# Optimization experiments

Hardware: AMD Instinct MI355X
Metric: run time of the kernel (lower is better)

The kernel has to match this reference:

```python
import math
import jax, jax.numpy as jnp
import numpy as np
from jax import lax

RADIUS = 3
KSIZE = 2 * RADIUS + 1  # 7
TOP_K = 8
SINKHORN_ITERS = 5


def _box_sum(x, h_axis, w_axis):
    # sum pooling with same padding over spatial axes
    wd = [1] * x.ndim
    wd[h_axis] = KSIZE
    wd[w_axis] = KSIZE
    pads = [(0, 0)] * x.ndim
    pads[h_axis] = (RADIUS, RADIUS)
    pads[w_axis] = (RADIUS, RADIUS)
    return lax.reduce_window(x, 0.0, lax.add, tuple(wd), (1,) * x.ndim, pads)


def geo_validate(src_pos, cand_pos, H, W):
    # src_pos [B,N,2], cand_pos [B,N,K,2] -> score [B,N,K]
    B, N, K, _ = cand_pos.shape
    src = src_pos.reshape(B, H, W, 1, 2)
    cand = cand_pos.reshape(B, H, W, K, 2)
    disp = cand - src  # [B,H,W,K,2]
    # count_include_pad=False -> divide by number of valid (in-bounds) taps
    cnt = _box_sum(jnp.ones((1, H, W, 1, 1), disp.dtype), 1, 2)
    mean = _box_sum(disp, 1, 2) / cnt
    mean_sq = _box_sum(disp * disp, 1, 2) / cnt
    var = jnp.clip(mean_sq - mean * mean, 0.0)
    total_var = var.sum(-1).reshape(B, N, K)
    return 1.0 / (1.0 + 100.0 * total_var)


def optimal_transport(scores, dustbin):
    B, M, N = scores.shape
    row = jnp.broadcast_to(dustbin, (B, M, 1))
    col = jnp.broadcast_to(dustbin, (B, 1, N))
    corner = jnp.zeros((B, 1, 1), scores.dtype)
    Z = jnp.concatenate([jnp.concatenate([scores, row], 2),
                         jnp.concatenate([col, corner], 2)], 1)  # [B,M+1,N+1]
    norm = -math.log(M + N)
    log_mu = jnp.full((M + 1,), norm, scores.dtype).at[M].set(math.log(N) + norm)
    log_nu = jnp.full((N + 1,), norm, scores.dtype).at[N].set(math.log(M) + norm)
    log_mu = jnp.broadcast_to(log_mu, (B, M + 1))
    log_nu = jnp.broadcast_to(log_nu, (B, N + 1))

    def body(_, uv):
        u, v = uv
        u = log_mu - jax.nn.logsumexp(Z + v[:, None, :], axis=2)
        v = log_nu - jax.nn.logsumexp(Z + u[:, :, None], axis=1)
        return (u, v)

    u0 = jnp.zeros((B, M + 1), scores.dtype)
    v0 = jnp.zeros((B, N + 1), scores.dtype)
    u, v = lax.fori_loop(0, SINKHORN_ITERS, body, (u0, v0))
    log_assign = Z + u[:, :, None] + v[:, None, :]
    return log_assign[:, :M, :N]


def solve_weighted_affine(src_pts, dst_pts, weights):
    # src/dst [B,N,2], weights [B,N,1] -> H_mat [B,3,3]
    B, N, _ = src_pts.shape
    w = weights[..., 0]
    w = w / jnp.clip(w.sum(1, keepdims=True), 1e-6)
    x, y = src_pts[..., 0], src_pts[..., 1]
    one = jnp.ones_like(x)
    zero = jnp.zeros_like(x)
    row_x = jnp.stack([x, y, one, zero, zero, zero], -1)   # [B,N,6]
    row_y = jnp.stack([zero, zero, zero, x, y, one], -1)
    A = jnp.concatenate([row_x, row_y], 1)                 # [B,2N,6]
    b = jnp.concatenate([dst_pts[..., 0], dst_pts[..., 1]], 1)[..., None]
    wd = jnp.concatenate([w, w], 1)[..., None]             # [B,2N,1]
    Aw = A * wd
    AtWA = jnp.einsum('bni,bnj->bij', Aw, A) + 1e-4 * jnp.eye(6, dtype=A.dtype)
    AtWb = jnp.einsum('bni,bnk->bik', Aw, b)
    p = jnp.linalg.solve(AtWA, AtWb)[..., 0]               # [B,6]
    a_, b_, c_, d_, e_, f_ = [p[:, i] for i in range(6)]
    z = jnp.zeros_like(a_)
    o = jnp.ones_like(a_)
    return jnp.stack([a_, b_, c_, d_, e_, f_, z, z, o], -1).reshape(B, 3, 3)


def matcher_forward(feat_A, feat_B, pos_A, pos_B, dustbin_score, geo_weight,
                    current_temp, H, W):
    B, N, C = feat_A.shape
    temp = current_temp[0]
    nA = feat_A / jnp.clip(jnp.linalg.norm(feat_A, axis=-1, keepdims=True), 1e-12)
    nB = feat_B / jnp.clip(jnp.linalg.norm(feat_B, axis=-1, keepdims=True), 1e-12)
    scores = jnp.einsum('bnc,bmc->bnm', nA, nB) / temp      # [B,N,N]
    log_assign = optimal_transport(scores, dustbin_score[0])
    ot_prob = jnp.exp(log_assign)
    topk_vals, topk_idx = lax.top_k(ot_prob, TOP_K)          # [B,N,K]
    bidx = jnp.arange(B)[:, None, None]
    topk_pos = pos_B[bidx, topk_idx]                         # [B,N,K,2]
    geo = geo_validate(pos_A, topk_pos, H, W)                # [B,N,K]
    gw = jnp.clip(geo_weight[0], 0.0, 2.0)
    combined = topk_vals + gw * geo
    soft = jax.nn.softmax(combined / temp, axis=-1)
    refined_warp = (topk_pos * soft[..., None]).sum(2)       # [B,N,2]
    conf = (soft * topk_vals).sum(-1, keepdims=True)         # [B,N,1]
    H_mat = solve_weighted_affine(pos_A, refined_warp, conf)
    return refined_warp, conf, H_mat


def setup_inputs() -> dict:
    key = jax.random.key(0)
    kA, kB, kP = jax.random.split(key, 3)
    B, H, W, C = 2, 64, 64, 128
    N = H * W
    feat_A = jax.random.normal(kA, (B, N, C), jnp.float32)
    feat_B = jax.random.normal(kB, (B, N, C), jnp.float32)
    # dense grid positions, normalized to [0,1]
    ys, xs = jnp.meshgrid(jnp.arange(H, dtype=jnp.float32),
                          jnp.arange(W, dtype=jnp.float32), indexing='ij')
    grid = jnp.stack([xs, ys], -1).reshape(1, N, 2) / float(max(H, W))
    pos_A = jnp.broadcast_to(grid, (B, N, 2))
    pos_B = pos_A + 0.01 * jax.random.normal(kP, (B, N, 2), jnp.float32)
    return {
        'feat_A': feat_A, 'feat_B': feat_B,
        'pos_A': pos_A, 'pos_B': pos_B,
        'dustbin_score': jnp.full((1,), -1.0, jnp.float32),
        'geo_weight': jnp.full((1,), 0.5, jnp.float32),
        'current_temp': jnp.full((1,), 0.1, jnp.float32),
        'H': H, 'W': W,
    }


def reference(feat_A, feat_B, pos_A, pos_B, dustbin_score, geo_weight,
              current_temp, H, W):
    return matcher_forward(feat_A, feat_B, pos_A, pos_B, dustbin_score,
                           geo_weight, current_temp, H, W)
```

## Files before the change

kernel.cpp:

```cpp
#include <hip/hip_runtime.h>
#include <math.h>

#define UVS 4104

#define OFF_ZU    33554432ul
#define OFF_WV    (OFF_ZU + 2*UVS)
#define OFF_RN    (OFF_WV + 2*UVS)
#define OFF_PARTS (OFF_RN + 16384)
#define OFF_TKV   (OFF_PARTS + 2097152)
#define OFF_TKP   (OFF_TKV + 65536)
#define OFF_DP    (OFF_TKP + 131072)
#define OFF_GEO   (OFF_DP + 131072)
#define OFF_SUM   (OFF_GEO + 65536)

#define EXPC    0.0001220703125f
#define HALFC   0.5f

#define PLANE   1048576

typedef __attribute__((ext_vector_type(8))) short bf16x8;
typedef __attribute__((ext_vector_type(4))) float f32x4;

static __device__ __forceinline__ unsigned f2bf(float x) {
    unsigned u = __float_as_uint(x);
    return (u + 0x7FFFu + ((u >> 16) & 1u)) >> 16;
}
static __device__ __forceinline__ float bf2f(unsigned h) { return __uint_as_float(h << 16); }

__global__ __launch_bounds__(256) void init_kernel(float* __restrict__ wv)
{
    int i = blockIdx.x * 256 + threadIdx.x;
    if (i < 2 * UVS) wv[i] = 1.0f;
}

__global__ __launch_bounds__(256) void norms_kernel(
    const float* __restrict__ fA, const float* __restrict__ fB, float* __restrict__ rn)
{
    int t = threadIdx.x;
    int rowg = blockIdx.x * 4 + (t >> 6);
    int lane = t & 63;
    const float* f = (rowg < 8192) ? fA : fB;
    int r = rowg & 8191;
    float x0 = f[(size_t)r * 128 + lane];
    float x1 = f[(size_t)r * 128 + 64 + lane];
    float s = x0 * x0 + x1 * x1;
    #pragma unroll
    for (int off = 32; off > 0; off >>= 1) s += __shfl_xor(s, off, 64);
    if (lane == 0) rn[rowg] = 1.f / fmaxf(sqrtf(s), 1e-12f);
}

__global__ __launch_bounds__(256) void pack_kernel(
    const float* __restrict__ fA, const float* __restrict__ fB, short* __restrict__ pk)
{
    int gt = blockIdx.x * 256 + threadIdx.x;
    int tensor = gt >> 17;
    int t = gt & 131071;
    int fr = t & 15;
    int kc = (t >> 4) & 15;
    int rb = (t >> 8) & 255;
    int b  = t >> 16;
    const float* src = tensor ? fB : fA;
    const float* p = src + ((size_t)(b * 4096 + rb * 16 + fr)) * 128 + kc * 8;
    float4 v0 = *(const float4*)p;
    float4 v1 = *(const float4*)(p + 4);
    float el[8] = {v0.x, v0.y, v0.z, v0.w, v1.x, v1.y, v1.z, v1.w};
    unsigned h[8], l[8];
    #pragma unroll
    for (int e = 0; e < 8; e++) { h[e] = f2bf(el[e]); l[e] = f2bf(el[e] - bf2f(h[e])); }
    uint4 hw = make_uint4(h[0] | (h[1] << 16), h[2] | (h[3] << 16),
                          h[4] | (h[5] << 16), h[6] | (h[7] << 16));
    uint4 lw = make_uint4(l[0] | (l[1] << 16), l[2] | (l[3] << 16),
                          l[4] | (l[5] << 16), l[6] | (l[7] << 16));
    size_t off = ((size_t)(b * 256 + rb)) * 2048 + kc * 128 + fr * 8;
    short* hi = pk + (size_t)tensor * 2 * PLANE;
    *(uint4*)(hi + off) = hw;
    *(uint4*)(hi + PLANE + off) = lw;
}

__global__ __launch_bounds__(256) void gemm_mfma(
    const short* __restrict__ pk, const float* __restrict__ rn,
    const float* __restrict__ temp, float* __restrict__ E0)
{
    __shared__ short Bs[16384];
    int b = blockIdx.z;
    int i0 = blockIdx.y * 64, j0 = blockIdx.x * 64;
    int t = threadIdx.x;
    int wave = t >> 6, lane = t & 63;
    int fr = lane & 15;
    int quad = lane >> 4;

    const short* gBhi = pk + 2 * (size_t)PLANE + ((size_t)(b * 256 + (j0 >> 4))) * 2048;
    const short* gBlo = gBhi + PLANE;
    #pragma unroll
    for (int c = 0; c < 4; c++) {
        int ch = c * 256 + t;
        *(uint4*)&Bs[ch * 8]        = *(const uint4*)(gBhi + ch * 8);
        *(uint4*)&Bs[8192 + ch * 8] = *(const uint4*)(gBlo + ch * 8);
    }

    const short* Abase_hi = pk + ((size_t)(b * 256 + (i0 >> 4) + wave)) * 2048;
    const short* Abase_lo = Abase_hi + PLANE;
    bf16x8 ah[4], al[4];
    #pragma unroll
    for (int s = 0; s < 4; s++) {
        ah[s] = *(const bf16x8*)(Abase_hi + s * 512 + lane * 8);
        al[s] = *(const bf16x8*)(Abase_lo + s * 512 + lane * 8);
    }
    __syncthreads();

    f32x4 acc[4] = {f32x4{0,0,0,0}, f32x4{0,0,0,0}, f32x4{0,0,0,0}, f32x4{0,0,0,0}};
    #pragma unroll
    for (int s = 0; s < 4; s++) {
        int lo = s * 512 + lane * 8;
        #pragma unroll
        for (int nb = 0; nb < 4; nb++) {
            bf16x8 bh = *(const bf16x8*)&Bs[nb * 2048 + lo];
            bf16x8 bl = *(const bf16x8*)&Bs[8192 + nb * 2048 + lo];
            acc[nb] = __builtin_amdgcn_mfma_f32_16x16x32_bf16(ah[s], bh, acc[nb], 0, 0, 0);
            acc[nb] = __builtin_amdgcn_mfma_f32_16x16x32_bf16(al[s], bh, acc[nb], 0, 0, 0);
            acc[nb] = __builtin_amdgcn_mfma_f32_16x16x32_bf16(ah[s], bl, acc[nb], 0, 0, 0);
        }
    }

    float invt = 1.f / temp[0];
    int m0 = i0 + wave * 16 + quad * 4;
    float ra[4];
    #pragma unroll
    for (int rr = 0; rr < 4; rr++) ra[rr] = rn[b * 4096 + m0 + rr] * invt;
    #pragma unroll
    for (int nb = 0; nb < 4; nb++) {
        int col = j0 + nb * 16 + fr;
        float rbv = rn[8192 + b * 4096 + col];
        #pragma unroll
        for (int rr = 0; rr < 4; rr++)
            E0[((size_t)(b * 4096 + m0 + rr)) * 4096 + col] = __expf(acc[nb][rr] * (ra[rr] * rbv));
    }
}

__global__ __launch_bounds__(256) void sink_fused(
    const float* __restrict__ E0, float* __restrict__ zu, const float* __restrict__ wv,
    const float* __restrict__ dbp, float* __restrict__ parts)
{
    int b = blockIdx.z;
    int t = threadIdx.x;
    int wave = t >> 6, lane = t & 63;
    int chb = blockIdx.x;
    const float* wb = wv + b * UVS;
    float edb = __expf(dbp[0]);
    __shared__ float S[4][4096];

    if (chb == 0 && wave == 0) {
        float sv = 0.f;
        #pragma unroll
        for (int c = 0; c < 16; c++) {
            f32x4 w4 = *(const f32x4*)(wb + lane * 4 + c * 256);
            sv += (w4.x + w4.y) + (w4.z + w4.w);
        }
        #pragma unroll
        for (int off = 32; off > 0; off >>= 1) sv += __shfl_xor(sv, off, 64);
        if (lane == 0) zu[b * UVS + 4096] = HALFC / (edb * sv + wb[4096]);
    }

    float dtail = edb * wb[4096];
    f32x4 cacc[16];
    #pragma unroll
    for (int c = 0; c < 16; c++) cacc[c] = f32x4{0, 0, 0, 0};

    const float* Eb = E0 + ((size_t)b << 24);
    int base = lane * 4;

    for (int r = 0; r < 4; r++) {
        int row = chb * 16 + wave * 4 + r;
        const float* Erow = Eb + ((size_t)row << 12);
        f32x4 x4[16];
        #pragma unroll
        for (int c = 0; c < 16; c++) x4[c] = *(const f32x4*)(Erow + base + c * 256);
        f32x4 rs4 = f32x4{0, 0, 0, 0};
        #pragma unroll
        for (int c = 0; c < 16; c++) {
            f32x4 w4 = *(const f32x4*)(wb + base + c * 256);
            rs4 += x4[c] * w4;
        }
        float rs = (rs4.x + rs4.y) + (rs4.z + rs4.w);
        #pragma unroll
        for (int off = 32; off > 0; off >>= 1) rs += __shfl_xor(rs, off, 64);
        float zi = EXPC / (rs + dtail);
        if (lane == 0) zu[b * UVS + row] = zi;
        #pragma unroll
        for (int c = 0; c < 16; c++) cacc[c] += x4[c] * zi;
    }

    #pragma unroll
    for (int c = 0; c < 16; c++) *(f32x4*)&S[wave][base + c * 256] = cacc[c];
    __syncthreads();
    float* pp = parts + ((size_t)(b * 256 + chb)) * 4096;
    #pragma unroll
    for (int k = 0; k < 16; k++) {
        int col = t + k * 256;
        pp[col] = (S[0][col] + S[1][col]) + (S[2][col] + S[3][col]);
    }
}

__global__ __launch_bounds__(256) void sink_vB(
    const float* __restrict__ parts, const float* __restrict__ zu,
    float* __restrict__ wv, const float* __restrict__ dbp)
{
    int b = blockIdx.z;
    int t = threadIdx.x;
    float edb = __expf(dbp[0]);
    if (blockIdx.x < 64) {
        int col = blockIdx.x * 64 + (t & 63);
        int grp = t >> 6;
        float s = 0.f;
        #pragma unroll 8
        for (int ch = grp * 64; ch < grp * 64 + 64; ch++)
            s += parts[((size_t)(b * 256 + ch)) * 4096 + col];
        __shared__ float red[4][64];
        red[grp][t & 63] = s;
        __syncthreads();
        if (grp == 0) {
            float tot = (red[0][t] + red[1][t]) + (red[2][t] + red[3][t]);
            tot += edb * zu[b * UVS + 4096];
            wv[b * UVS + col] = EXPC / tot;
        }
    } else {
        __shared__ float red2[256];
        float s = 0.f;
        for (int i = t; i < 4096; i += 256) s += zu[b * UVS + i];
        red2[t] = s; __syncthreads();
        for (int off = 128; off > 0; off >>= 1) {
            if (t < off) red2[t] += red2[t + off];
            __syncthreads();
        }
        if (t == 0)
            wv[b * UVS + 4096] = HALFC / (edb * red2[0] + zu[b * UVS + 4096]);
    }
}

#define FCMPSWAP(a, b) { float _mx = fmaxf(a, b), _mn = fminf(a, b); (a) = _mx; (b) = _mn; }
__global__ __launch_bounds__(256) void topk_kernel(
    const float* __restrict__ E0, const float* __restrict__ zu, const float* __restrict__ wv,
    const float* __restrict__ posA, const float* __restrict__ posB,
    float* __restrict__ tkv, float* __restrict__ tkp, float* __restrict__ dp)
{
    int wave = threadIdx.x >> 6;
    int lane = threadIdx.x & 63;
    int row = blockIdx.x * 4 + wave;
    int b = row >> 12; int i = row & 4095;
    const float* Erow = E0 + (size_t)row * 4096;
    const float* wb = wv + b * UVS;

    __shared__ unsigned long long cand[4][64];
    __shared__ int ccnt[4];
    if (lane == 0) ccnt[wave] = 0;

    f32x4 q[16];
    #pragma unroll
    for (int c = 0; c < 16; c++) {
        int j = c * 256 + lane * 4;
        f32x4 x = *(const f32x4*)(Erow + j);
        f32x4 w = *(const f32x4*)(wb + j);
        q[c] = x * w;
    }
    __builtin_amdgcn_sched_barrier(0);

    float s[8] = {0, 0, 0, 0, 0, 0, 0, 0};
    #pragma unroll
    for (int c = 0; c < 16; c++) {
        float el[4] = {q[c].x, q[c].y, q[c].z, q[c].w};
        #pragma unroll
        for (int e = 0; e < 4; e++) {
            float xv = el[e];
            s[7] = __builtin_amdgcn_fmed3f(s[6], s[7], xv);
            s[6] = __builtin_amdgcn_fmed3f(s[5], s[6], xv);
            s[5] = __builtin_amdgcn_fmed3f(s[4], s[5], xv);
            s[4] = __builtin_amdgcn_fmed3f(s[3], s[4], xv);
            s[3] = __builtin_amdgcn_fmed3f(s[2], s[3], xv);
            s[2] = __builtin_amdgcn_fmed3f(s[1], s[2], xv);
            s[1] = __builtin_amdgcn_fmed3f(s[0], s[1], xv);
            s[0] = fmaxf(s[0], xv);
        }
    }

    #pragma unroll
    for (int st = 0; st < 6; st++) {
        int off = 1 << st;
        float o[8];
        #pragma unroll
        for (int r = 0; r < 8; r++) o[r] = __shfl_xor(s[r], off, 64);
        float m[8];
        #pragma unroll
        for (int r = 0; r < 8; r++) m[r] = fmaxf(s[r], o[7 - r]);
        FCMPSWAP(m[0], m[4]); FCMPSWAP(m[1], m[5]); FCMPSWAP(m[2], m[6]); FCMPSWAP(m[3], m[7]);
        FCMPSWAP(m[0], m[2]); FCMPSWAP(m[1], m[3]); FCMPSWAP(m[4], m[6]); FCMPSWAP(m[5], m[7]);
        FCMPSWAP(m[0], m[1]); FCMPSWAP(m[2], m[3]); FCMPSWAP(m[4], m[5]); FCMPSWAP(m[6], m[7]);
        #pragma unroll
        for (int r = 0; r < 8; r++) s[r] = m[r];
    }
    float t8 = s[7];

    __syncthreads();

    #pragma unroll
    for (int c = 0; c < 16; c++) {
        float el[4] = {q[c].x, q[c].y, q[c].z, q[c].w};
        #pragma unroll
        for (int e = 0; e < 4; e++) {
            if (el[e] >= t8) {
                int j = c * 256 + lane * 4 + e;
                unsigned long long key =
                    ((unsigned long long)__float_as_uint(el[e]) << 32) | (unsigned)(4095 - j);
                int slot = atomicAdd(&ccnt[wave], 1);
                if (slot < 64) cand[wave][slot] = key;
            }
        }
    }
    __syncthreads();

    int cnt = ccnt[wave]; if (cnt > 64) cnt = 64;
    if (lane < cnt) {
        unsigned long long my = cand[wave][lane];
        int rank = 0;
        for (int j2 = 0; j2 < cnt; j2++) rank += (cand[wave][j2] > my) ? 1 : 0;
        if (rank < 8) {
            int idx = 4095 - (int)(my & 0xFFFFFFFFu);
            float candv = __uint_as_float((unsigned)(my >> 32));
            float val = candv * zu[b * UVS + i];
            float px = posB[((size_t)(b * 4096 + idx)) * 2 + 0];
            float py = posB[((size_t)(b * 4096 + idx)) * 2 + 1];
            float ax = posA[((size_t)(b * 4096 + i)) * 2 + 0];
            float ay = posA[((size_t)(b * 4096 + i)) * 2 + 1];
            size_t base = ((size_t)(b * 4096 + i)) * 8 + rank;
            tkv[base] = val;
            tkp[base * 2 + 0] = px; tkp[base * 2 + 1] = py;
            dp[((size_t)((b * 8 + rank) * 2 + 0)) * 4096 + i] = px - ax;
            dp[((size_t)((b * 8 + rank) * 2 + 1)) * 4096 + i] = py - ay;
        }
    }
}

__global__ __launch_bounds__(256) void geo_kernel(
    const float* __restrict__ dp, float* __restrict__ geo)
{
    int tid = blockIdx.x * 256 + threadIdx.x;
    int n = tid & 4095; int bk = tid >> 12;
    int b = bk >> 3; int k = bk & 7;
    int h = n >> 6, w = n & 63;
    const float* dpx = dp + ((size_t)(bk * 2 + 0)) * 4096;
    const float* dpy = dp + ((size_t)(bk * 2 + 1)) * 4096;
    float sx = 0, sy = 0, sxx = 0, syy = 0, cnt = 0;
    #pragma unroll
    for (int dy = -3; dy <= 3; dy++) {
        int hh = h + dy; if ((unsigned)hh >= 64u) continue;
        #pragma unroll
        for (int dx = -3; dx <= 3; dx++) {
            int ww = w + dx; if ((unsigned)ww >= 64u) continue;
            int nn = (hh << 6) + ww;
            float vx = dpx[nn], vy = dpy[nn];
            sx += vx; sy += vy; sxx += vx * vx; syy += vy * vy; cnt += 1.f;
        }
    }
    float inv = 1.f / cnt;
    float mx = sx * inv, my = sy * inv;
    float varx = fmaxf(sxx * inv - mx * mx, 0.f);
    float vary = fmaxf(syy * inv - my * my, 0.f);
    geo[((size_t)(b * 4096 + n)) * 8 + k] = 1.f / (1.f + 100.f * (varx + vary));
}

__global__ __launch_bounds__(256) void refine_kernel(
    const float* __restrict__ tkv, const float* __restrict__ geo,
    const float* __restrict__ tkp, const float* __restrict__ gwp,
    const float* __restrict__ tpp, float* __restrict__ out)
{
    int tid = blockIdx.x * 256 + threadIdx.x;
    float gw = fminf(fmaxf(gwp[0], 0.f), 2.f);
    float invt = 1.f / tpp[0];
    size_t base = (size_t)tid * 8;
    float cb[8], vv[8];
    float mx = -INFINITY;
    #pragma unroll
    for (int k = 0; k < 8; k++) { vv[k] = tkv[base + k]; cb[k] = vv[k] + gw * geo[base + k]; mx = fmaxf(mx, cb[k]); }
    float e[8], se = 0;
    #pragma unroll
    for (int k = 0; k < 8; k++) { e[k] = __expf((cb[k] - mx) * invt); se += e[k]; }
    float wx = 0, wy = 0, cf = 0; float inv = 1.f / se;
    #pragma unroll
    for (int k = 0; k < 8; k++) {
        float s = e[k] * inv;
        wx += s * tkp[(base + k) * 2 + 0];
        wy += s * tkp[(base + k) * 2 + 1];
        cf += s * vv[k];
    }
    out[(size_t)tid * 2 + 0] = wx;
    out[(size_t)tid * 2 + 1] = wy;
    out[16384 + tid] = cf;
}

__global__ __launch_bounds__(256) void affine_reduce(
    const float* __restrict__ posA, const float* __restrict__ out, double* __restrict__ sums)
{
    int b = blockIdx.x; int t = threadIdx.x;
    double acc[12] = {0,0,0,0,0,0,0,0,0,0,0,0};
    for (int n = t; n < 4096; n += 256) {
        size_t idx = (size_t)b * 4096 + n;
        float x = posA[idx * 2], y = posA[idx * 2 + 1];
        float dx = out[idx * 2], dy = out[idx * 2 + 1];
        float c = out[16384 + idx];
        double cd = (double)c;
        double cx = cd * x, cy = cd * y;
        acc[0] += cx * x;  acc[1] += cx * y;  acc[2] += cy * y;
        acc[3] += cx;      acc[4] += cy;      acc[5] += cd;
        acc[6] += cx * dx; acc[7] += cy * dx; acc[8] += cd * dx;
        acc[9] += cx * dy; acc[10] += cy * dy; acc[11] += cd * dy;
    }
    __shared__ double red[256];
    for (int s = 0; s < 12; s++) {
        red[t] = acc[s]; __syncthreads();
        for (int off = 128; off > 0; off >>= 1) {
            if (t < off) red[t] += red[t + off];
            __syncthreads();
        }
        if (t == 0) sums[b * 12 + s] = red[0];
        __syncthreads();
    }
}

__global__ void affine_solve(const double* __restrict__ sums, float* __restrict__ out)
{
    int t = threadIdx.x;
    if (t >= 2) return;
    int b = t;
    const double* s = sums + b * 12;
    double den = s[5] > 1e-6 ? s[5] : 1e-6;
    double g00 = s[0] / den + 1e-4, g01 = s[1] / den, g02 = s[3] / den;
    double g11 = s[2] / den + 1e-4, g12 = s[4] / den;
    double g22 = s[5] / den + 1e-4;
    double bx0 = s[6] / den, bx1 = s[7] / den, bx2 = s[8] / den;
    double by0 = s[9] / den, by1 = s[10] / den, by2 = s[11] / den;
    double c00 = g11 * g22 - g12 * g12;
    double c01 = g02 * g12 - g01 * g22;
    double c02 = g01 * g12 - g02 * g11;
    double det = g00 * c00 + g01 * c01 + g02 * c02;
    double id = 1.0 / det;
    double i00 = c00 * id, i01 = c01 * id, i02 = c02 * id;
    double i11 = (g00 * g22 - g02 * g02) * id, i12 = (g01 * g02 - g00 * g12) * id;
    double i22 = (g00 * g11 - g01 * g01) * id;
    double a_ = i00 * bx0 + i01 * bx1 + i02 * bx2;
    double b_ = i01 * bx0 + i11 * bx1 + i12 * bx2;
    double c_ = i02 * bx0 + i12 * bx1 + i22 * bx2;
    double d_ = i00 * by0 + i01 * by1 + i02 * by2;
    double e_ = i01 * by0 + i11 * by1 + i12 * by2;
    double f_ = i02 * by0 + i12 * by1 + i22 * by2;
    float* o = out + 24576 + b * 9;
    o[0] = (float)a_; o[1] = (float)b_; o[2] = (float)c_;
    o[3] = (float)d_; o[4] = (float)e_; o[5] = (float)f_;
    o[6] = 0.f; o[7] = 0.f; o[8] = 1.f;
}

extern "C" void kernel_launch(void* const* d_in, const int* in_sizes, int n_in,
                              void* d_out, int out_size, void* d_ws, size_t ws_size,
                              hipStream_t stream) {
    const float* fA = (const float*)d_in[0];
    const float* fB = (const float*)d_in[1];
    const float* pA = (const float*)d_in[2];
    const float* pB = (const float*)d_in[3];
    const float* db = (const float*)d_in[4];
    const float* gw = (const float*)d_in[5];
    const float* tp = (const float*)d_in[6];

    float* ws    = (float*)d_ws;
    float* out   = (float*)d_out;
    float* E0    = ws;
    float* zu    = ws + OFF_ZU;
    float* wv    = ws + OFF_WV;
    float* rn    = ws + OFF_RN;
    float* parts = ws + OFF_PARTS;
    short* pk    = (short*)(ws + OFF_PARTS);
    float* tkv   = ws + OFF_TKV;
    float* tkp   = ws + OFF_TKP;
    float* dp    = ws + OFF_DP;
    float* geo   = ws + OFF_GEO;
    double* sums = (double*)(ws + OFF_SUM);

    init_kernel<<<33, 256, 0, stream>>>(wv);
    norms_kernel<<<4096, 256, 0, stream>>>(fA, fB, rn);
    pack_kernel<<<1024, 256, 0, stream>>>(fA, fB, pk);
    gemm_mfma<<<dim3(64, 64, 2), 256, 0, stream>>>(pk, rn, tp, E0);

    for (int it = 0; it < 5; it++) {
        sink_fused<<<dim3(256, 1, 2), 256, 0, stream>>>(E0, zu, wv, db, parts);
        sink_vB<<<dim3(65, 1, 2), 256, 0, stream>>>(parts, zu, wv, db);
    }

    topk_kernel<<<2048, 256, 0, stream>>>(E0, zu, wv, pA, pB, tkv, tkp, dp);
    geo_kernel<<<256, 256, 0, stream>>>(dp, geo);
    refine_kernel<<<32, 256, 0, stream>>>(tkv, geo, tkp, gw, tp, out);
    affine_reduce<<<2, 256, 0, stream>>>(pA, out, sums);
    affine_solve<<<1, 64, 0, stream>>>(sums, out);
}
```

Baseline: 323.2 us.

## Double-buffer row loads in sinkhorn kernel and split top-k rows across whole block

The sinkhorn row-scaling kernel now prefetches the next row's 16 vector loads into a second register buffer while computing the current row, overlapping global loads with the dot product and accumulation. The top-k kernel now assigns one row per 256-thread block instead of one row per wave. Each thread scans 16 elements instead of 64, and per-wave top-8 lists are merged in shared memory to find the threshold. This shortens the serial per-thread sort chain and raises parallelism, at the cost of more register pressure in sinkhorn, four times as many top-k blocks, and an extra block-level barrier and merge step.

Result: slower. 358.6 us (+11.0%).

```diff
diff --git a/kernel.cpp b/kernel.cpp
--- a/kernel.cpp
+++ b/kernel.cpp
@@ -168,27 +168,44 @@
 
     const float* Eb = E0 + ((size_t)b << 24);
     int base = lane * 4;
-
-    for (int r = 0; r < 4; r++) {
-        int row = chb * 16 + wave * 4 + r;
-        const float* Erow = Eb + ((size_t)row << 12);
-        f32x4 x4[16];
-        #pragma unroll
-        for (int c = 0; c < 16; c++) x4[c] = *(const f32x4*)(Erow + base + c * 256);
-        f32x4 rs4 = f32x4{0, 0, 0, 0};
-        #pragma unroll
-        for (int c = 0; c < 16; c++) {
-            f32x4 w4 = *(const f32x4*)(wb + base + c * 256);
-            rs4 += x4[c] * w4;
-        }
-        float rs = (rs4.x + rs4.y) + (rs4.z + rs4.w);
-        #pragma unroll
-        for (int off = 32; off > 0; off >>= 1) rs += __shfl_xor(rs, off, 64);
-        float zi = EXPC / (rs + dtail);
-        if (lane == 0) zu[b * UVS + row] = zi;
-        #pragma unroll
-        for (int c = 0; c < 16; c++) cacc[c] += x4[c] * zi;
-    }
+    int row0 = chb * 16 + wave * 4;
+
+    f32x4 xa[16], xb[16];
+    {
+        const float* Er = Eb + ((size_t)row0 << 12);
+        #pragma unroll
+        for (int c = 0; c < 16; c++) xa[c] = *(const f32x4*)(Er + base + c * 256);
+    }
+
+#define SINK_ROW(BUF, NXT, ROW, PREF)                                          \
+    {                                                                          \
+        if (PREF) {                                                            \
+            const float* Ern = Eb + ((size_t)((ROW) + 1) << 12);               \
+            _Pragma("unroll")                                                  \
+            for (int c = 0; c < 16; c++)                                       \
+                NXT[c] = *(const f32x4*)(Ern + base + c * 256);                \
+        }                                                                      \
+        __builtin_amdgcn_sched_barrier(0);                                     \
+        f32x4 rs4 = f32x4{0, 0, 0, 0};                                         \
+        _Pragma("unroll")                                                      \
+        for (int c = 0; c < 16; c++) {                                         \
+            f32x4 w4 = *(const f32x4*)(wb + base + c * 256);                   \
+            rs4 += BUF[c] * w4;                                                \
+        }                                                                      \
+        float rs = (rs4.x + rs4.y) + (rs4.z + rs4.w);                          \
+        _Pragma("unroll")                                                      \
+        for (int off = 32; off > 0; off >>= 1) rs += __shfl_xor(rs, off, 64);  \
+        float zi = EXPC / (rs + dtail);                                        \
+        if (lane == 0) zu[b * UVS + (ROW)] = zi;                               \
+        _Pragma("unroll")                                                      \
+        for (int c = 0; c < 16; c++) cacc[c] += BUF[c] * zi;                   \
+    }
+
+    SINK_ROW(xa, xb, row0 + 0, 1)
+    SINK_ROW(xb, xa, row0 + 1, 1)
+    SINK_ROW(xa, xb, row0 + 2, 1)
+    SINK_ROW(xb, xa, row0 + 3, 0)
+#undef SINK_ROW
 
     #pragma unroll
     for (int c = 0; c < 16; c++) *(f32x4*)&S[wave][base + c * 256] = cacc[c];
@@ -243,21 +260,23 @@
     const float* __restrict__ posA, const float* __restrict__ posB,
     float* __restrict__ tkv, float* __restrict__ tkp, float* __restrict__ dp)
 {
-    int wave = threadIdx.x >> 6;
-    int lane = threadIdx.x & 63;
-    int row = blockIdx.x * 4 + wave;
+    int row = blockIdx.x;
+    int t = threadIdx.x;
+    int wave = t >> 6, lane = t & 63;
     int b = row >> 12; int i = row & 4095;
     const float* Erow = E0 + (size_t)row * 4096;
     const float* wb = wv + b * UVS;
 
-    __shared__ unsigned long long cand[4][64];
-    __shared__ int ccnt[4];
-    if (lane == 0) ccnt[wave] = 0;
-
-    f32x4 q[16];
-    #pragma unroll
-    for (int c = 0; c < 16; c++) {
-        int j = c * 256 + lane * 4;
+    __shared__ float sv32[32];
+    __shared__ float t8s;
+    __shared__ unsigned long long cand[64];
+    __shared__ int ccnt;
+    if (t == 0) ccnt = 0;
+
+    f32x4 q[4];
+    #pragma unroll
+    for (int c = 0; c < 4; c++) {
+        int j = t * 4 + c * 1024;
         f32x4 x = *(const f32x4*)(Erow + j);
         f32x4 w = *(const f32x4*)(wb + j);
         q[c] = x * w;
@@ -266,7 +285,7 @@
 
     float s[8] = {0, 0, 0, 0, 0, 0, 0, 0};
     #pragma unroll
-    for (int c = 0; c < 16; c++) {
+    for (int c = 0; c < 4; c++) {
         float el[4] = {q[c].x, q[c].y, q[c].z, q[c].w};
         #pragma unroll
         for (int e = 0; e < 4; e++) {
@@ -297,31 +316,46 @@
         #pragma unroll
         for (int r = 0; r < 8; r++) s[r] = m[r];
     }
-    float t8 = s[7];
-
+    if (lane == 0) {
+        #pragma unroll
+        for (int r = 0; r < 8; r++) sv32[wave * 8 + r] = s[r];
+    }
     __syncthreads();
 
-    #pragma unroll
-    for (int c = 0; c < 16; c++) {
+    if (t < 32) {
+        float my = sv32[t];
+        int rank = 0;
+        #pragma unroll
+        for (int k = 0; k < 32; k++) {
+            float vk = sv32[k];
+            rank += (vk > my || (vk == my && k < t)) ? 1 : 0;
+        }
+        if (rank == 7) t8s = my;
+    }
+    __syncthreads();
+    float t8 = t8s;
+
+    #pragma unroll
+    for (int c = 0; c < 4; c++) {
         float el[4] = {q[c].x, q[c].y, q[c].z, q[c].w};
         #pragma unroll
         for (int e = 0; e < 4; e++) {
             if (el[e] >= t8) {
-                int j = c * 256 + lane * 4 + e;
+                int j = t * 4 + c * 1024 + e;
                 unsigned long long key =
                     ((unsigned long long)__float_as_uint(el[e]) << 32) | (unsigned)(4095 - j);
-                int slot = atomicAdd(&ccnt[wave], 1);
-                if (slot < 64) cand[wave][slot] = key;
+                int slot = atomicAdd(&ccnt, 1);
+                if (slot < 64) cand[slot] = key;
             }
         }
     }
     __syncthreads();
 
-    int cnt = ccnt[wave]; if (cnt > 64) cnt = 64;
-    if (lane < cnt) {
-        unsigned long long my = cand[wave][lane];
+    int cnt = ccnt; if (cnt > 64) cnt = 64;
+    if (t < cnt) {
+        unsigned long long my = cand[t];
         int rank = 0;
-        for (int j2 = 0; j2 < cnt; j2++) rank += (cand[wave][j2] > my) ? 1 : 0;
+        for (int j2 = 0; j2 < cnt; j2++) rank += (cand[j2] > my) ? 1 : 0;
         if (rank < 8) {
             int idx = 4095 - (int)(my & 0xFFFFFFFFu);
             float candv = __uint_as_float((unsigned)(my >> 32));
@@ -492,7 +526,7 @@
         sink_vB<<<dim3(65, 1, 2), 256, 0, stream>>>(parts, zu, wv, db);
     }
 
-    topk_kernel<<<2048, 256, 0, stream>>>(E0, zu, wv, pA, pB, tkv, tkp, dp);
+    topk_kernel<<<8192, 256, 0, stream>>>(E0, zu, wv, pA, pB, tkv, tkp, dp);
     geo_kernel<<<256, 256, 0, stream>>>(dp, geo);
     refine_kernel<<<32, 256, 0, stream>>>(tkv, geo, tkp, gw, tp, out);
     affine_reduce<<<2, 256, 0, stream>>>(pA, out, sums);
```

## Split Sinkhorn row pass across waves per row, quadruple grid blocks

Applied to the files above, without the earlier changes.

Each sink_fused block now handles 4 rows with all four waves sharing each row across column quarters, instead of 16 rows with each wave owning full rows. This drops the 64KB shared-memory buffer and the large per-thread register arrays, so occupancy should rise and the grid becomes 1024 blocks per batch. The cost is four times more partial column sums (parts grows to 1024 rows per batch), which sink_vB must read and reduce with a wider block layout.

New measurement: 357.6 us. 10.6% more time.

```diff
diff --git a/kernel.cpp b/kernel.cpp
--- a/kernel.cpp
+++ b/kernel.cpp
@@ -7,7 +7,7 @@
 #define OFF_WV    (OFF_ZU + 2*UVS)
 #define OFF_RN    (OFF_WV + 2*UVS)
 #define OFF_PARTS (OFF_RN + 16384)
-#define OFF_TKV   (OFF_PARTS + 2097152)
+#define OFF_TKV   (OFF_PARTS + 8388608)
 #define OFF_TKP   (OFF_TKV + 65536)
 #define OFF_DP    (OFF_TKP + 131072)
 #define OFF_GEO   (OFF_DP + 131072)
@@ -147,7 +147,7 @@
     int chb = blockIdx.x;
     const float* wb = wv + b * UVS;
     float edb = __expf(dbp[0]);
-    __shared__ float S[4][4096];
+    __shared__ float rsum[16];
 
     if (chb == 0 && wave == 0) {
         float sv = 0.f;
@@ -162,42 +162,52 @@
     }
 
     float dtail = edb * wb[4096];
-    f32x4 cacc[16];
-    #pragma unroll
-    for (int c = 0; c < 16; c++) cacc[c] = f32x4{0, 0, 0, 0};
-
     const float* Eb = E0 + ((size_t)b << 24);
-    int base = lane * 4;
-
+    int off0 = wave * 1024 + lane * 4;
+    int row0 = chb * 4;
+
+    f32x4 wreg[4];
+    #pragma unroll
+    for (int c = 0; c < 4; c++) wreg[c] = *(const f32x4*)(wb + off0 + c * 256);
+
+    f32x4 x[4][4];
+    #pragma unroll
     for (int r = 0; r < 4; r++) {
-        int row = chb * 16 + wave * 4 + r;
-        const float* Erow = Eb + ((size_t)row << 12);
-        f32x4 x4[16];
-        #pragma unroll
-        for (int c = 0; c < 16; c++) x4[c] = *(const f32x4*)(Erow + base + c * 256);
-        f32x4 rs4 = f32x4{0, 0, 0, 0};
-        #pragma unroll
-        for (int c = 0; c < 16; c++) {
-            f32x4 w4 = *(const f32x4*)(wb + base + c * 256);
-            rs4 += x4[c] * w4;
-        }
-        float rs = (rs4.x + rs4.y) + (rs4.z + rs4.w);
-        #pragma unroll
-        for (int off = 32; off > 0; off >>= 1) rs += __shfl_xor(rs, off, 64);
-        float zi = EXPC / (rs + dtail);
-        if (lane == 0) zu[b * UVS + row] = zi;
-        #pragma unroll
-        for (int c = 0; c < 16; c++) cacc[c] += x4[c] * zi;
-    }
-
-    #pragma unroll
-    for (int c = 0; c < 16; c++) *(f32x4*)&S[wave][base + c * 256] = cacc[c];
+        const float* Erow = Eb + ((size_t)(row0 + r) << 12);
+        f32x4 ps4 = f32x4{0, 0, 0, 0};
+        #pragma unroll
+        for (int c = 0; c < 4; c++) {
+            x[r][c] = *(const f32x4*)(Erow + off0 + c * 256);
+            ps4 += x[r][c] * wreg[c];
+        }
+        float ps = (ps4.x + ps4.y) + (ps4.z + ps4.w);
+        #pragma unroll
+        for (int off = 32; off > 0; off >>= 1) ps += __shfl_xor(ps, off, 64);
+        if (lane == 0) rsum[r * 4 + wave] = ps;
+    }
     __syncthreads();
-    float* pp = parts + ((size_t)(b * 256 + chb)) * 4096;
-    #pragma unroll
-    for (int k = 0; k < 16; k++) {
-        int col = t + k * 256;
-        pp[col] = (S[0][col] + S[1][col]) + (S[2][col] + S[3][col]);
+
+    float z[4];
+    #pragma unroll
+    for (int r = 0; r < 4; r++) {
+        float srow = (rsum[r * 4 + 0] + rsum[r * 4 + 1]) + (rsum[r * 4 + 2] + rsum[r * 4 + 3]);
+        z[r] = EXPC / (srow + dtail);
+    }
+    if (t == 0) {
+        zu[b * UVS + row0 + 0] = z[0];
+        zu[b * UVS + row0 + 1] = z[1];
+        zu[b * UVS + row0 + 2] = z[2];
+        zu[b * UVS + row0 + 3] = z[3];
+    }
+
+    float* pp = parts + ((size_t)(b * 1024 + chb)) * 4096 + off0;
+    #pragma unroll
+    for (int c = 0; c < 4; c++) {
+        f32x4 acc = x[0][c] * z[0];
+        acc += x[1][c] * z[1];
+        acc += x[2][c] * z[2];
+        acc += x[3][c] * z[3];
+        *(f32x4*)(pp + c * 256) = acc;
     }
 }
 
@@ -208,18 +218,20 @@
     int b = blockIdx.z;
     int t = threadIdx.x;
     float edb = __expf(dbp[0]);
-    if (blockIdx.x < 64) {
-        int col = blockIdx.x * 64 + (t & 63);
-        int grp = t >> 6;
+    if (blockIdx.x < 256) {
+        int col = blockIdx.x * 16 + (t & 15);
+        int grp = t >> 4;
         float s = 0.f;
         #pragma unroll 8
         for (int ch = grp * 64; ch < grp * 64 + 64; ch++)
-            s += parts[((size_t)(b * 256 + ch)) * 4096 + col];
-        __shared__ float red[4][64];
-        red[grp][t & 63] = s;
+            s += parts[((size_t)(b * 1024 + ch)) * 4096 + col];
+        __shared__ float red[16][16];
+        red[grp][t & 15] = s;
         __syncthreads();
         if (grp == 0) {
-            float tot = (red[0][t] + red[1][t]) + (red[2][t] + red[3][t]);
+            float tot = 0.f;
+            #pragma unroll
+            for (int g = 0; g < 16; g++) tot += red[g][t];
             tot += edb * zu[b * UVS + 4096];
             wv[b * UVS + col] = EXPC / tot;
         }
@@ -488,8 +500,8 @@
     gemm_mfma<<<dim3(64, 64, 2), 256, 0, stream>>>(pk, rn, tp, E0);
 
     for (int it = 0; it < 5; it++) {
-        sink_fused<<<dim3(256, 1, 2), 256, 0, stream>>>(E0, zu, wv, db, parts);
-        sink_vB<<<dim3(65, 1, 2), 256, 0, stream>>>(parts, zu, wv, db);
+        sink_fused<<<dim3(1024, 1, 2), 256, 0, stream>>>(E0, zu, wv, db, parts);
+        sink_vB<<<dim3(257, 1, 2), 256, 0, stream>>>(parts, zu, wv, db);
     }
 
     topk_kernel<<<2048, 256, 0, stream>>>(E0, zu, wv, pA, pB, tkv, tkp, dp);
```
